# Performance work log

Measured on AMD Instinct MI355X. Metric: run time of the kernel, lower is better.

## Reference

```python
import jax, jax.numpy as jnp
import numpy as np

B, N_DET, N_T, NY, NX = 4, 128, 2048, 256, 256


def setup_inputs() -> dict:
    key = jax.random.key(0)
    k1, k2, k3 = jax.random.split(key, 3)
    sino = jax.random.normal(k1, (B, 1, N_DET, N_T), dtype=jnp.float32)
    # LUT channel 0: floor temporal index (stored as float, cast to int in forward)
    k_floor = jax.random.randint(k2, (NY, NX, N_DET), 0, N_T).astype(jnp.float32)
    # LUT channel 1: linear interpolation weight alpha in [0,1)
    alpha = jax.random.uniform(k3, (NY, NX, N_DET), dtype=jnp.float32)
    lut = jnp.stack([k_floor, alpha], axis=-1)  # [NY, NX, N_DET, 2]
    return {"sino": sino, "lut": lut}


def reference(sino, lut):
    # sino: [B, 1, n_det, n_t]; lut: [ny, nx, n_det, 2]
    b, c, n_det, n_t = sino.shape
    k_floor = lut[..., 0].astype(jnp.int32)          # [ny, nx, n_det]
    alpha = lut[..., 1]                               # [ny, nx, n_det]
    valid = (k_floor >= 0) & (k_floor < n_t - 1)
    k0 = jnp.clip(k_floor, 0, n_t - 2)
    k1 = k0 + 1
    S = sino[:, 0]                                    # [B, n_det, n_t]
    det = jnp.arange(n_det)                           # broadcasts against [ny,nx,n_det]
    s0 = S[:, det, k0]                                # [B, ny, nx, n_det]
    s1 = S[:, det, k1]                                # [B, ny, nx, n_det]
    sk = (1.0 - alpha) * s0 + alpha * s1
    sk = jnp.where(valid, sk, jnp.zeros_like(sk))
    # Hann apodization window over detectors
    apod = (0.5 - 0.5 * jnp.cos(2.0 * jnp.pi * jnp.arange(n_det, dtype=jnp.float32)
                                / max(n_det - 1, 1))).astype(sino.dtype)
    out = jnp.einsum('bijd,d->bij', sk, apod)
    norm = jnp.maximum(apod.sum(), 1e-06)
    out = out / norm
    return out[:, None]                               # [B, 1, ny, nx]
```

## Files before the change

### kernel.cpp

```cpp
#include <hip/hip_runtime.h>
#include <hip/hip_fp16.h>


#define NB      4
#define NDET    128
#define NT      2048
#define NPIX    65536
#define DBLOCK  8
#define THREADS 256

__global__ __launch_bounds__(256)
void cvt_kernel(const float* __restrict__ sino, uint2* __restrict__ ws16) {
    const int id = blockIdx.x * 256 + threadIdx.x;
    float v0 = sino[id];
    float v1 = sino[id + NDET * NT];
    float v2 = sino[id + 2 * NDET * NT];
    float v3 = sino[id + 3 * NDET * NT];
    __half2 h01 = __floats2half2_rn(v0, v1);
    __half2 h23 = __floats2half2_rn(v2, v3);
    uint2 u;
    u.x = *(const unsigned*)&h01;
    u.y = *(const unsigned*)&h23;
    ws16[id] = u;
}

__global__ __launch_bounds__(THREADS, 4)
void bp_kernel(const uint2* __restrict__ ws16,
               const float* __restrict__ lut,
               float* __restrict__ out) {
    const int tid   = threadIdx.x;
    const int octet = blockIdx.x & 15;
    const int px    = (blockIdx.x >> 4) * THREADS + tid;
    const int d0    = octet * DBLOCK;

    float apod[DBLOCK];
#pragma unroll
    for (int j = 0; j < DBLOCK; ++j) {
        float x = (float)(d0 + j) * (6.28318530717958647692f / 127.0f);
        apod[j] = 0.5f - 0.5f * __cosf(x);
    }

    const float4* lp = (const float4*)(lut + ((size_t)px * NDET + d0) * 2);
    float4 L[4];
#pragma unroll
    for (int q = 0; q < 4; ++q) L[q] = lp[q];

    int   k0v[DBLOCK];
    float afv[DBLOCK], wv[DBLOCK];
#pragma unroll
    for (int q = 0; q < 4; ++q) {
#pragma unroll
        for (int h = 0; h < 2; ++h) {
            int   j  = q * 2 + h;
            float kf = h ? L[q].z : L[q].x;
            float af = h ? L[q].w : L[q].y;
            int k = (int)kf;
            bool valid = (unsigned)k < (unsigned)(NT - 1);
            k0v[j] = valid ? k : 0;
            afv[j] = af;
            wv[j]  = valid ? apod[j] : 0.0f;
        }
    }

    uint2 e0[DBLOCK], e1[DBLOCK];
#pragma unroll
    for (int j = 0; j < DBLOCK; ++j) {
        const uint2* row = ws16 + (size_t)(d0 + j) * NT;
        e0[j] = row[k0v[j]];
        e1[j] = row[k0v[j] + 1];
    }

    float acc[NB] = {0.0f, 0.0f, 0.0f, 0.0f};
#pragma unroll
    for (int j = 0; j < DBLOCK; ++j) {
        __half2 a01 = *(__half2*)&e0[j].x, a23 = *(__half2*)&e0[j].y;
        __half2 b01 = *(__half2*)&e1[j].x, b23 = *(__half2*)&e1[j].y;
        __half2 a2  = __float2half2_rn(afv[j]);
        __half2 s01 = __hfma2(a2, __hsub2(b01, a01), a01);
        __half2 s23 = __hfma2(a2, __hsub2(b23, a23), a23);
        float2 f01 = __half22float2(s01);
        float2 f23 = __half22float2(s23);
        acc[0] = fmaf(wv[j], f01.x, acc[0]);
        acc[1] = fmaf(wv[j], f01.y, acc[1]);
        acc[2] = fmaf(wv[j], f23.x, acc[2]);
        acc[3] = fmaf(wv[j], f23.y, acc[3]);
    }

    const float inv_norm = 1.0f / 63.5f;
#pragma unroll
    for (int b = 0; b < NB; ++b)
        atomicAdd(&out[(size_t)b * NPIX + px], acc[b] * inv_norm);
}

__global__ __launch_bounds__(512, 4)
void bp_fallback(const float* __restrict__ sino,
                 const float* __restrict__ lut,
                 float* __restrict__ out) {
    __shared__ __half2 lds[4][NT];
    const int tid   = threadIdx.x;
    const int octet = blockIdx.x & 15;
    const int tile  = blockIdx.x >> 4;
    const int d0    = octet * DBLOCK;
    const int px0   = tile * 1024;
    float apod[DBLOCK];
#pragma unroll
    for (int j = 0; j < DBLOCK; ++j) {
        float x = (float)(d0 + j) * (6.28318530717958647692f / 127.0f);
        apod[j] = 0.5f - 0.5f * __cosf(x);
    }
    float4 L[2][4];
#pragma unroll
    for (int i = 0; i < 2; ++i) {
        const float4* lq = (const float4*)
            (lut + ((size_t)(px0 + tid + i * 512) * NDET + d0) * 2);
#pragma unroll
        for (int q = 0; q < 4; ++q) L[i][q] = lq[q];
    }
    float acc[2][NB];
#pragma unroll
    for (int i = 0; i < 2; ++i)
#pragma unroll
        for (int b = 0; b < NB; ++b) acc[i][b] = 0.0f;
    const float4* s4 = (const float4*)sino;
    for (int ph = 0; ph < 4; ++ph) {
        const int b0  = (ph >> 1) * 2;
        const int dh  = ph & 1;
        const int dg0 = d0 + dh * 4;
        if (ph) __syncthreads();
        for (int f = tid; f < 4 * (NT / 4); f += 512) {
            int dl = f >> 9;
            int t4 = f & 511;
            size_t row = ((size_t)b0 * NDET + dg0 + dl) * (NT / 4) + t4;
            float4 ve = s4[row];
            float4 vo = s4[row + (size_t)NDET * (NT / 4)];
            __half2* dstp = &lds[dl][t4 * 4];
            dstp[0] = __floats2half2_rn(ve.x, vo.x);
            dstp[1] = __floats2half2_rn(ve.y, vo.y);
            dstp[2] = __floats2half2_rn(ve.z, vo.z);
            dstp[3] = __floats2half2_rn(ve.w, vo.w);
        }
        __syncthreads();
#pragma unroll
        for (int i = 0; i < 2; ++i) {
#pragma unroll
            for (int q2 = 0; q2 < 2; ++q2) {
                float4 Lq = L[i][dh * 2 + q2];
#pragma unroll
                for (int h = 0; h < 2; ++h) {
                    float kf = h ? Lq.z : Lq.x;
                    float af = h ? Lq.w : Lq.y;
                    int   dl = q2 * 2 + h;
                    int k = (int)kf;
                    bool valid = (unsigned)k < (unsigned)(NT - 1);
                    float w  = valid ? apod[dh * 4 + dl] : 0.0f;
                    int  k0  = valid ? k : 0;
                    __half2 s0v = lds[dl][k0];
                    __half2 s1v = lds[dl][k0 + 1];
                    __half2 a2  = __float2half2_rn(af);
                    __half2 sk  = __hfma2(a2, __hsub2(s1v, s0v), s0v);
                    float2  fv  = __half22float2(sk);
                    acc[i][b0 + 0] = fmaf(w, fv.x, acc[i][b0 + 0]);
                    acc[i][b0 + 1] = fmaf(w, fv.y, acc[i][b0 + 1]);
                }
            }
        }
    }
    const float inv_norm = 1.0f / 63.5f;
#pragma unroll
    for (int i = 0; i < 2; ++i) {
        const int px = px0 + tid + i * 512;
#pragma unroll
        for (int b = 0; b < NB; ++b)
            atomicAdd(&out[(size_t)b * NPIX + px], acc[i][b] * inv_norm);
    }
}

extern "C" void kernel_launch(void* const* d_in, const int* in_sizes, int n_in,
                              void* d_out, int out_size, void* d_ws, size_t ws_size,
                              hipStream_t stream) {
    const float* sino = (const float*)d_in[0];
    const float* lut  = (const float*)d_in[1];
    float* out = (float*)d_out;

    (void)hipMemsetAsync(d_out, 0, (size_t)out_size * sizeof(float), stream);

    const size_t ws_needed = (size_t)NDET * NT * sizeof(uint2);
    if (ws_size >= ws_needed) {
        uint2* ws16 = (uint2*)d_ws;
        cvt_kernel<<<dim3(NDET * NT / 256), dim3(256), 0, stream>>>(sino, ws16);
        bp_kernel<<<dim3(4096), dim3(THREADS), 0, stream>>>(ws16, lut, out);
    } else {
        bp_fallback<<<dim3(1024), dim3(512), 0, stream>>>(sino, lut, out);
    }
}
```

Baseline: 128.3 us.

## Map detector octets to lanes and reduce via wave shuffles instead of atomics

```diff
diff --git a/kernel.cpp b/kernel.cpp
--- a/kernel.cpp
+++ b/kernel.cpp
@@ -6,7 +6,6 @@
 #define NDET    128
 #define NT      2048
 #define NPIX    65536
-#define DBLOCK  8
 #define THREADS 256
 
 __global__ __launch_bounds__(256)
@@ -28,25 +27,27 @@
 void bp_kernel(const uint2* __restrict__ ws16,
                const float* __restrict__ lut,
                float* __restrict__ out) {
-    const int tid   = threadIdx.x;
-    const int octet = blockIdx.x & 15;
-    const int px    = (blockIdx.x >> 4) * THREADS + tid;
-    const int d0    = octet * DBLOCK;
+    const int tid    = threadIdx.x;
+    const int lane   = tid & 63;
+    const int wid    = tid >> 6;
+    const int octet  = lane & 15;
+    const int px_sub = lane >> 4;
+    const int px     = blockIdx.x * 16 + wid * 4 + px_sub;
+    const int d0     = octet * 8;
 
-    float apod[DBLOCK];
+    float apod[8];
 #pragma unroll
-    for (int j = 0; j < DBLOCK; ++j) {
+    for (int j = 0; j < 8; ++j) {
         float x = (float)(d0 + j) * (6.28318530717958647692f / 127.0f);
         apod[j] = 0.5f - 0.5f * __cosf(x);
     }
 
-    const float4* lp = (const float4*)(lut + ((size_t)px * NDET + d0) * 2);
+    const float4* lp = (const float4*)lut + ((size_t)px * 64 + octet * 4);
     float4 L[4];
 #pragma unroll
     for (int q = 0; q < 4; ++q) L[q] = lp[q];
 
-    int   k0v[DBLOCK];
-    float afv[DBLOCK], wv[DBLOCK];
+    float acc[NB] = {0.0f, 0.0f, 0.0f, 0.0f};
 #pragma unroll
     for (int q = 0; q < 4; ++q) {
 #pragma unroll
@@ -56,40 +57,38 @@
             float af = h ? L[q].w : L[q].y;
             int k = (int)kf;
             bool valid = (unsigned)k < (unsigned)(NT - 1);
-            k0v[j] = valid ? k : 0;
-            afv[j] = af;
-            wv[j]  = valid ? apod[j] : 0.0f;
+            float w  = valid ? apod[j] : 0.0f;
+            int  k0  = valid ? k : 0;
+            const uint2* row = ws16 + (size_t)(d0 + j) * NT + k0;
+            uint2 e0 = row[0];
+            uint2 e1 = row[1];
+            __half2 a01 = *(__half2*)&e0.x, a23 = *(__half2*)&e0.y;
+            __half2 b01 = *(__half2*)&e1.x, b23 = *(__half2*)&e1.y;
+            __half2 a2  = __float2half2_rn(af);
+            __half2 s01 = __hfma2(a2, __hsub2(b01, a01), a01);
+            __half2 s23 = __hfma2(a2, __hsub2(b23, a23), a23);
+            float2 f01 = __half22float2(s01);
+            float2 f23 = __half22float2(s23);
+            acc[0] = fmaf(w, f01.x, acc[0]);
+            acc[1] = fmaf(w, f01.y, acc[1]);
+            acc[2] = fmaf(w, f23.x, acc[2]);
+            acc[3] = fmaf(w, f23.y, acc[3]);
         }
     }
 
-    uint2 e0[DBLOCK], e1[DBLOCK];
 #pragma unroll
-    for (int j = 0; j < DBLOCK; ++j) {
-        const uint2* row = ws16 + (size_t)(d0 + j) * NT;
-        e0[j] = row[k0v[j]];
-        e1[j] = row[k0v[j] + 1];
+    for (int m = 1; m < 16; m <<= 1) {
+#pragma unroll
+        for (int b = 0; b < NB; ++b)
+            acc[b] += __shfl_xor(acc[b], m, 64);
     }
 
-    float acc[NB] = {0.0f, 0.0f, 0.0f, 0.0f};
+    if (octet == 0) {
+        const float inv_norm = 1.0f / 63.5f;
 #pragma unroll
-    for (int j = 0; j < DBLOCK; ++j) {
-        __half2 a01 = *(__half2*)&e0[j].x, a23 = *(__half2*)&e0[j].y;
-        __half2 b01 = *(__half2*)&e1[j].x, b23 = *(__half2*)&e1[j].y;
-        __half2 a2  = __float2half2_rn(afv[j]);
-        __half2 s01 = __hfma2(a2, __hsub2(b01, a01), a01);
-        __half2 s23 = __hfma2(a2, __hsub2(b23, a23), a23);
-        float2 f01 = __half22float2(s01);
-        float2 f23 = __half22float2(s23);
-        acc[0] = fmaf(wv[j], f01.x, acc[0]);
-        acc[1] = fmaf(wv[j], f01.y, acc[1]);
-        acc[2] = fmaf(wv[j], f23.x, acc[2]);
-        acc[3] = fmaf(wv[j], f23.y, acc[3]);
+        for (int b = 0; b < NB; ++b)
+            out[(size_t)b * NPIX + px] = acc[b] * inv_norm;
     }
-
-    const float inv_norm = 1.0f / 63.5f;
-#pragma unroll
-    for (int b = 0; b < NB; ++b)
-        atomicAdd(&out[(size_t)b * NPIX + px], acc[b] * inv_norm);
 }
 
 __global__ __launch_bounds__(512, 4)
@@ -100,11 +99,11 @@
     const int tid   = threadIdx.x;
     const int octet = blockIdx.x & 15;
     const int tile  = blockIdx.x >> 4;
-    const int d0    = octet * DBLOCK;
+    const int d0    = octet * 8;
     const int px0   = tile * 1024;
-    float apod[DBLOCK];
+    float apod[8];
 #pragma unroll
-    for (int j = 0; j < DBLOCK; ++j) {
+    for (int j = 0; j < 8; ++j) {
         float x = (float)(d0 + j) * (6.28318530717958647692f / 127.0f);
         apod[j] = 0.5f - 0.5f * __cosf(x);
     }
@@ -182,14 +181,13 @@
     const float* lut  = (const float*)d_in[1];
     float* out = (float*)d_out;
 
-    (void)hipMemsetAsync(d_out, 0, (size_t)out_size * sizeof(float), stream);
-
     const size_t ws_needed = (size_t)NDET * NT * sizeof(uint2);
     if (ws_size >= ws_needed) {
         uint2* ws16 = (uint2*)d_ws;
         cvt_kernel<<<dim3(NDET * NT / 256), dim3(256), 0, stream>>>(sino, ws16);
-        bp_kernel<<<dim3(4096), dim3(THREADS), 0, stream>>>(ws16, lut, out);
+        bp_kernel<<<dim3(NPIX / 16), dim3(THREADS), 0, stream>>>(ws16, lut, out);
     } else {
+        (void)hipMemsetAsync(d_out, 0, (size_t)out_size * sizeof(float), stream);
         bp_fallback<<<dim3(1024), dim3(512), 0, stream>>>(sino, lut, out);
     }
 }
```

Result: no change. 125.9 us (-1.9%).
